# Optimization experiments

Hardware: AMD Instinct MI355X
Metric: run time of the kernel (lower is better)

## Reference

```python
import jax, jax.numpy as jnp
import numpy as np

NEG_SLOPE = 0.01  # nn.LeakyReLU default


def leaky_relu(x):
    return jnp.where(x >= 0, x, NEG_SLOPE * x)


def gcn_conv(x, W, b, src, dst, n_nodes):
    """PyG GCNConv: add self loops, symmetric D^-1/2 (A+I) D^-1/2 norm, then x @ W + b."""
    h = x @ W  # [N, D]
    # degree with self-loops (edge weight 1 each, +1 for the self loop)
    deg = jnp.zeros((n_nodes,), dtype=x.dtype).at[dst].add(1.0) + 1.0
    dinv = jax.lax.rsqrt(deg)  # deg >= 1 thanks to self loops
    norm = dinv[src] * dinv[dst]  # [E]
    msg = h[src] * norm[:, None]  # gather + scale, [E, D]
    agg = jnp.zeros_like(h).at[dst].add(msg)  # scatter-add over targets
    agg = agg + h * (dinv * dinv)[:, None]  # self-loop contribution
    return agg + b


def setup_inputs() -> dict:
    key = jax.random.key(0)
    ks = jax.random.split(key, 12)
    N, E = 100000, 640000
    ND, D, C = 239, 128, 2
    x = jax.random.normal(ks[0], (N, ND), dtype=jnp.float32)
    edge_index = jax.random.randint(ks[1], (2, E), 0, N, dtype=jnp.int64)
    edge_type = jax.random.randint(ks[2], (E,), 0, 4, dtype=jnp.int64)
    s = 0.05
    W_in = jax.random.normal(ks[3], (ND, D), dtype=jnp.float32) * s
    b_in = jax.random.normal(ks[4], (D,), dtype=jnp.float32) * s
    W_g = jax.random.normal(ks[5], (D, D), dtype=jnp.float32) * s
    b_g = jax.random.normal(ks[6], (D,), dtype=jnp.float32) * s
    W_o1 = jax.random.normal(ks[7], (D, D), dtype=jnp.float32) * s
    b_o1 = jax.random.normal(ks[8], (D,), dtype=jnp.float32) * s
    W_o2 = jax.random.normal(ks[9], (D, C), dtype=jnp.float32) * s
    b_o2 = jax.random.normal(ks[10], (C,), dtype=jnp.float32) * s
    return {"x": x, "edge_index": edge_index, "edge_type": edge_type,
            "W_in": W_in, "b_in": b_in, "W_g": W_g, "b_g": b_g,
            "W_o1": W_o1, "b_o1": b_o1, "W_o2": W_o2, "b_o2": b_o2}


def reference(x, edge_index, edge_type, W_in, b_in, W_g, b_g, W_o1, b_o1, W_o2, b_o2):
    n_nodes = x.shape[0]
    src, dst = edge_index[0], edge_index[1]
    h = leaky_relu(x @ W_in + b_in)
    h = gcn_conv(h, W_g, b_g, src, dst, n_nodes)
    # dropout is identity in eval mode (training=False)
    h = gcn_conv(h, W_g, b_g, src, dst, n_nodes)  # same shared GCNConv instance
    h = leaky_relu(h @ W_o1 + b_o1)
    return h @ W_o2 + b_o2
```

## Files before the change

kernel.cpp:

```cpp
#include <hip/hip_runtime.h>
#include <hip/hip_bf16.h>


typedef __attribute__((ext_vector_type(8))) __bf16 bf16x8;
typedef __attribute__((ext_vector_type(4))) float f32x4;

typedef __attribute__((address_space(1))) const void gvoid_t;
typedef __attribute__((address_space(3))) void svoid_t;

__global__ __launch_bounds__(256) void wtr_all_k(const float* __restrict__ W_in,
                                                 const float* __restrict__ W_g,
                                                 const float* __restrict__ W_o1,
                                                 ushort* __restrict__ Wt_in,
                                                 ushort* __restrict__ Wt_g,
                                                 ushort* __restrict__ Wt_o1, int ND) {
  int idx = blockIdx.x * 256 + threadIdx.x;
  if (idx < 128 * 256) {
    int n = idx >> 8, k = idx & 255;
    float v = (k < ND) ? W_in[(size_t)k * 128 + n] : 0.f;
    __hip_bfloat16 h = __float2bfloat16(v);
    Wt_in[idx] = *(ushort*)&h;
  } else if (idx < 128 * 256 + 128 * 128) {
    int j = idx - 128 * 256;
    int n = j >> 7, k = j & 127;
    __hip_bfloat16 h = __float2bfloat16(W_g[(size_t)k * 128 + n]);
    Wt_g[j] = *(ushort*)&h;
  } else if (idx < 128 * 256 + 2 * 128 * 128) {
    int j = idx - 128 * 256 - 128 * 128;
    int n = j >> 7, k = j & 127;
    __hip_bfloat16 h = __float2bfloat16(W_o1[(size_t)k * 128 + n]);
    Wt_o1[j] = *(ushort*)&h;
  }
}


__global__ __launch_bounds__(256) void zero_k(int* __restrict__ p, int n) {
  int i = blockIdx.x * 256 + threadIdx.x;
  if (i < n) p[i] = 0;
}

__global__ __launch_bounds__(256) void hist_k(const int* __restrict__ dst, int* __restrict__ cnt, int E) {
  int e = blockIdx.x * 256 + threadIdx.x;
  if (e < E) atomicAdd(&cnt[dst[e]], 1);
}

__global__ __launch_bounds__(256) void scan1_k(const int* __restrict__ cnt, int* __restrict__ rp,
                                               int* __restrict__ bsum, int N) {
  __shared__ int sd[256];
  int t = threadIdx.x;
  int base = blockIdx.x * 1024 + t * 4;
  int v0 = (base + 0 < N) ? cnt[base + 0] : 0;
  int v1 = (base + 1 < N) ? cnt[base + 1] : 0;
  int v2 = (base + 2 < N) ? cnt[base + 2] : 0;
  int v3 = (base + 3 < N) ? cnt[base + 3] : 0;
  int ts = v0 + v1 + v2 + v3;
  sd[t] = ts;
  __syncthreads();
  for (int off = 1; off < 256; off <<= 1) {
    int y = (t >= off) ? sd[t - off] : 0;
    __syncthreads();
    sd[t] += y;
    __syncthreads();
  }
  int x = sd[t] - ts;
  if (t == 255) bsum[blockIdx.x] = sd[255];
  if (base + 0 < N) rp[base + 0] = x; x += v0;
  if (base + 1 < N) rp[base + 1] = x; x += v1;
  if (base + 2 < N) rp[base + 2] = x; x += v2;
  if (base + 3 < N) rp[base + 3] = x;
}

__global__ __launch_bounds__(256) void scan2_k(int* __restrict__ bsum, int NB) {
  __shared__ int sd[256];
  int t = threadIdx.x;
  int base = t * 4;
  int v0 = (base + 0 < NB) ? bsum[base + 0] : 0;
  int v1 = (base + 1 < NB) ? bsum[base + 1] : 0;
  int v2 = (base + 2 < NB) ? bsum[base + 2] : 0;
  int v3 = (base + 3 < NB) ? bsum[base + 3] : 0;
  int ts = v0 + v1 + v2 + v3;
  sd[t] = ts;
  __syncthreads();
  for (int off = 1; off < 256; off <<= 1) {
    int y = (t >= off) ? sd[t - off] : 0;
    __syncthreads();
    sd[t] += y;
    __syncthreads();
  }
  int x = sd[t] - ts;
  if (base + 0 < NB) bsum[base + 0] = x; x += v0;
  if (base + 1 < NB) bsum[base + 1] = x; x += v1;
  if (base + 2 < NB) bsum[base + 2] = x; x += v2;
  if (base + 3 < NB) bsum[base + 3] = x;
}

__global__ __launch_bounds__(256) void scan3_k(int* __restrict__ rp, int* __restrict__ pos,
                                               const int* __restrict__ bsum,
                                               float* __restrict__ dinv, int N, int E) {
  int i = blockIdx.x * 256 + threadIdx.x;
  if (i < N) {
    int c = pos[i];
    int v = rp[i] + bsum[i >> 10];
    dinv[i] = rsqrtf((float)c + 1.0f);
    rp[i] = v;
    pos[i] = v;
  }
  if (i == 0) rp[N] = E;
}

__global__ __launch_bounds__(256) void fill_k(const int* __restrict__ src, const int* __restrict__ dst,
                                              const float* __restrict__ dinv,
                                              int* __restrict__ pos, int2* __restrict__ ew, int E) {
  int e = blockIdx.x * 256 + threadIdx.x;
  if (e < E) {
    int d = dst[e];
    int s = src[e];
    int idx = atomicAdd(&pos[d], 1);
    ew[idx] = make_int2(s, __float_as_int(dinv[s] * dinv[d]));
  }
}


__global__ __launch_bounds__(512, 4) void gemm1_k(const float* __restrict__ x,
                                                  const ushort* __restrict__ Wt,
                                                  const float* __restrict__ bias,
                                                  ushort* __restrict__ C, int N, int Ka) {
  __shared__ float Af[64 * 239 + 8];
  __shared__ ushort Wl[128 * 72];
  const int tid = threadIdx.x;
  const int wave = tid >> 6;
  const int lane = tid & 63;
  const int l16 = lane & 15;
  const int quad = lane >> 4;
  const int m0 = blockIdx.x * 64;

  {
    int rows = N - m0;
    if (rows > 64) rows = 64;
    const int nwords = rows * Ka;
    const float* __restrict__ gsrc = x + (size_t)m0 * Ka;
    const int nchunks = nwords >> 8;
    for (int ch = wave; ch < nchunks; ch += 8) {
      __builtin_amdgcn_global_load_lds(
          (gvoid_t*)(gsrc + ch * 256 + lane * 4),
          (svoid_t*)(&Af[ch * 256]), 16, 0, 0);
    }
    for (int i = (nchunks << 8) + tid; i < nwords; i += 512) {
      Af[i] = gsrc[i];
    }
  }

  f32x4 acc[4] = {};
  const int wr = wave >> 1;
  const int wc = wave & 1;
  const int wn = tid >> 2;
  const int wseg = tid & 3;
#pragma unroll
  for (int kc = 0; kc < 4; ++kc) {
    __syncthreads();
    *(uint4*)&Wl[wn * 72 + wseg * 16] =
        *(const uint4*)(Wt + (size_t)wn * 256 + kc * 64 + wseg * 16);
    *(uint4*)&Wl[wn * 72 + wseg * 16 + 8] =
        *(const uint4*)(Wt + (size_t)wn * 256 + kc * 64 + wseg * 16 + 8);
    __syncthreads();
#pragma unroll
    for (int s = 0; s < 2; ++s) {
      const int koff = kc * 64 + s * 32 + quad * 8;
      bf16x8 a = {};
      const float* ap = &Af[(wr * 16 + l16) * Ka + koff];
      if (koff + 8 <= Ka) {
#pragma unroll
        for (int j = 0; j < 8; ++j) {
          __hip_bfloat16 h = __float2bfloat16(ap[j]);
          a[j] = *(__bf16*)&h;
        }
      } else if (koff < Ka) {
#pragma unroll
        for (int j = 0; j < 8; ++j) {
          if (koff + j < Ka) {
            __hip_bfloat16 h = __float2bfloat16(ap[j]);
            a[j] = *(__bf16*)&h;
          }
        }
      }
      const int wof = s * 32 + quad * 8;
#pragma unroll
      for (int c = 0; c < 4; ++c) {
        bf16x8 b = *(const bf16x8*)&Wl[(wc * 64 + c * 16 + l16) * 72 + wof];
        acc[c] = __builtin_amdgcn_mfma_f32_16x16x32_bf16(a, b, acc[c], 0, 0, 0);
      }
    }
  }

  float bv[4];
#pragma unroll
  for (int c = 0; c < 4; ++c) bv[c] = bias[wc * 64 + c * 16 + l16];
#pragma unroll
  for (int reg = 0; reg < 4; ++reg) {
    int row = m0 + wr * 16 + quad * 4 + reg;
    if (row < N) {
#pragma unroll
      for (int c = 0; c < 4; ++c) {
        float v = acc[c][reg] + bv[c];
        v = v >= 0.f ? v : 0.01f * v;
        __hip_bfloat16 h = __float2bfloat16(v);
        C[(size_t)row * 128 + wc * 64 + c * 16 + l16] = *(ushort*)&h;
      }
    }
  }
}


template <int MODE>
__global__ __launch_bounds__(512, 4) void mgemm_k(const ushort* __restrict__ A,
                                                  const ushort* __restrict__ Wt,
                                                  const float* __restrict__ bias,
                                                  const float* __restrict__ W2,
                                                  const float* __restrict__ b2,
                                                  void* __restrict__ C, int N) {
  __shared__ uint4 Al[128 * 16];
  __shared__ uint4 Wl[128 * 16];
  const int tid = threadIdx.x;
  const int wave = tid >> 6;
  const int lane = tid & 63;
  const int l16 = lane & 15;
  const int quad = lane >> 4;
  const int m0 = blockIdx.x * 128;

  f32x4 acc[8] = {};
  const int r_s = tid >> 4;
  const int j8 = tid & 15;
#pragma unroll
  for (int it = 0; it < 4; ++it) {
    int m = it * 32 + r_s;
    Al[m * 16 + (j8 ^ (m & 15))] = *(const uint4*)(A + (size_t)(m0 + m) * 128 + j8 * 8);
  }
#pragma unroll
  for (int it = 0; it < 4; ++it) {
    int n = it * 32 + r_s;
    Wl[n * 16 + (j8 ^ (n & 15))] = *(const uint4*)(Wt + (size_t)n * 128 + j8 * 8);
  }
  __syncthreads();
#pragma unroll
  for (int s = 0; s < 4; ++s) {
    const int j = s * 4 + quad;
    const int arow = wave * 16 + l16;
    bf16x8 a = *(const bf16x8*)&Al[arow * 16 + (j ^ (arow & 15))];
#pragma unroll
    for (int c = 0; c < 8; ++c) {
      const int brow = c * 16 + l16;
      bf16x8 b = *(const bf16x8*)&Wl[brow * 16 + (j ^ (brow & 15))];
      acc[c] = __builtin_amdgcn_mfma_f32_16x16x32_bf16(a, b, acc[c], 0, 0, 0);
    }
  }

  float bv[8];
#pragma unroll
  for (int c = 0; c < 8; ++c) bv[c] = bias[c * 16 + l16];

  if constexpr (MODE == 3) {
    float w20[8], w21[8];
#pragma unroll
    for (int c = 0; c < 8; ++c) {
      int colj = c * 16 + l16;
      w20[c] = W2[colj * 2 + 0];
      w21[c] = W2[colj * 2 + 1];
    }
    float bb0 = b2[0], bb1 = b2[1];
#pragma unroll
    for (int reg = 0; reg < 4; ++reg) {
      float o0 = 0.f, o1 = 0.f;
#pragma unroll
      for (int c = 0; c < 8; ++c) {
        float v = acc[c][reg] + bv[c];
        v = v >= 0.f ? v : 0.01f * v;
        o0 = fmaf(v, w20[c], o0);
        o1 = fmaf(v, w21[c], o1);
      }
      o0 += __shfl_xor(o0, 1); o0 += __shfl_xor(o0, 2);
      o0 += __shfl_xor(o0, 4); o0 += __shfl_xor(o0, 8);
      o1 += __shfl_xor(o1, 1); o1 += __shfl_xor(o1, 2);
      o1 += __shfl_xor(o1, 4); o1 += __shfl_xor(o1, 8);
      int row = m0 + wave * 16 + quad * 4 + reg;
      if (l16 == 0 && row < N)
        *(float2*)((float*)C + (size_t)row * 2) = make_float2(o0 + bb0, o1 + bb1);
    }
    return;
  }

#pragma unroll
  for (int reg = 0; reg < 4; ++reg) {
    int row = m0 + wave * 16 + quad * 4 + reg;
    if (row < N) {
#pragma unroll
      for (int c = 0; c < 8; ++c) {
        float v = acc[c][reg] + bv[c];
        __hip_bfloat16 h = __float2bfloat16(v);
        ((ushort*)C)[(size_t)row * 128 + c * 16 + l16] = *(ushort*)&h;
      }
    }
  }
}


__global__ __launch_bounds__(256) void agg_k(const ushort* __restrict__ T,
                                             const float* __restrict__ dinv,
                                             const int* __restrict__ rp,
                                             const int2* __restrict__ ew,
                                             ushort* __restrict__ O, int N) {
  int l = threadIdx.x & 15;
  int node = blockIdx.x * 16 + (threadIdx.x >> 4);
  if (node >= N) return;
  float di = dinv[node];
  float dsq = di * di;
  const uint4* T4 = (const uint4*)T;
  float a[8];
  {
    uint4 sv = T4[(size_t)node * 16 + l];
    uint u[4] = {sv.x, sv.y, sv.z, sv.w};
#pragma unroll
    for (int p = 0; p < 4; ++p) {
      a[2 * p + 0] = __uint_as_float(u[p] << 16) * dsq;
      a[2 * p + 1] = __uint_as_float(u[p] & 0xFFFF0000u) * dsq;
    }
  }
  int e = rp[node];
  const int e1 = rp[node + 1];
  for (; e + 4 <= e1; e += 4) {
    int2 p0 = ew[e + 0], p1 = ew[e + 1], p2 = ew[e + 2], p3 = ew[e + 3];
    uint4 v0 = T4[(size_t)p0.x * 16 + l];
    uint4 v1 = T4[(size_t)p1.x * 16 + l];
    uint4 v2 = T4[(size_t)p2.x * 16 + l];
    uint4 v3 = T4[(size_t)p3.x * 16 + l];
    float w0 = __int_as_float(p0.y), w1 = __int_as_float(p1.y);
    float w2 = __int_as_float(p2.y), w3 = __int_as_float(p3.y);
    uint u0[4] = {v0.x, v0.y, v0.z, v0.w};
    uint u1[4] = {v1.x, v1.y, v1.z, v1.w};
    uint u2[4] = {v2.x, v2.y, v2.z, v2.w};
    uint u3[4] = {v3.x, v3.y, v3.z, v3.w};
#pragma unroll
    for (int p = 0; p < 4; ++p) {
      a[2 * p + 0] = fmaf(__uint_as_float(u0[p] << 16), w0, a[2 * p + 0]);
      a[2 * p + 1] = fmaf(__uint_as_float(u0[p] & 0xFFFF0000u), w0, a[2 * p + 1]);
      a[2 * p + 0] = fmaf(__uint_as_float(u1[p] << 16), w1, a[2 * p + 0]);
      a[2 * p + 1] = fmaf(__uint_as_float(u1[p] & 0xFFFF0000u), w1, a[2 * p + 1]);
      a[2 * p + 0] = fmaf(__uint_as_float(u2[p] << 16), w2, a[2 * p + 0]);
      a[2 * p + 1] = fmaf(__uint_as_float(u2[p] & 0xFFFF0000u), w2, a[2 * p + 1]);
      a[2 * p + 0] = fmaf(__uint_as_float(u3[p] << 16), w3, a[2 * p + 0]);
      a[2 * p + 1] = fmaf(__uint_as_float(u3[p] & 0xFFFF0000u), w3, a[2 * p + 1]);
    }
  }
  if (e + 2 <= e1) {
    int2 p0 = ew[e + 0], p1 = ew[e + 1];
    uint4 v0 = T4[(size_t)p0.x * 16 + l];
    uint4 v1 = T4[(size_t)p1.x * 16 + l];
    float w0 = __int_as_float(p0.y), w1 = __int_as_float(p1.y);
    uint u0[4] = {v0.x, v0.y, v0.z, v0.w};
    uint u1[4] = {v1.x, v1.y, v1.z, v1.w};
#pragma unroll
    for (int p = 0; p < 4; ++p) {
      a[2 * p + 0] = fmaf(__uint_as_float(u0[p] << 16), w0, a[2 * p + 0]);
      a[2 * p + 1] = fmaf(__uint_as_float(u0[p] & 0xFFFF0000u), w0, a[2 * p + 1]);
      a[2 * p + 0] = fmaf(__uint_as_float(u1[p] << 16), w1, a[2 * p + 0]);
      a[2 * p + 1] = fmaf(__uint_as_float(u1[p] & 0xFFFF0000u), w1, a[2 * p + 1]);
    }
    e += 2;
  }
  if (e < e1) {
    int2 pw = ew[e];
    float w = __int_as_float(pw.y);
    uint4 v = T4[(size_t)pw.x * 16 + l];
    uint u[4] = {v.x, v.y, v.z, v.w};
#pragma unroll
    for (int p = 0; p < 4; ++p) {
      a[2 * p + 0] = fmaf(__uint_as_float(u[p] << 16), w, a[2 * p + 0]);
      a[2 * p + 1] = fmaf(__uint_as_float(u[p] & 0xFFFF0000u), w, a[2 * p + 1]);
    }
  }
  union { uint4 v; ushort s[8]; } uo;
#pragma unroll
  for (int j = 0; j < 8; ++j) {
    __hip_bfloat16 h = __float2bfloat16(a[j]);
    uo.s[j] = *(ushort*)&h;
  }
  ((uint4*)O)[(size_t)node * 16 + l] = uo.v;
}


extern "C" void kernel_launch(void* const* d_in, const int* in_sizes, int n_in,
                              void* d_out, int out_size, void* d_ws, size_t ws_size,
                              hipStream_t stream) {
  const float* x = (const float*)d_in[0];
  const int* ei = (const int*)d_in[1];
  const float* W_in = (const float*)d_in[3];
  const float* b_in = (const float*)d_in[4];
  const float* W_g  = (const float*)d_in[5];
  const float* b_g  = (const float*)d_in[6];
  const float* W_o1 = (const float*)d_in[7];
  const float* b_o1 = (const float*)d_in[8];
  const float* W_o2 = (const float*)d_in[9];
  const float* b_o2 = (const float*)d_in[10];

  const int D = in_sizes[4];
  const int ND = in_sizes[3] / D;
  const int N = in_sizes[0] / ND;
  const int E = in_sizes[2];
  const int* src = ei;
  const int* dst = ei + E;

  const int N_pad = ((N + 127) / 128) * 128;
  const size_t np = (size_t)N_pad;
  const int KP1 = 256;

  ushort* hA = (ushort*)d_ws;
  ushort* hB = hA + np * 128;
  ushort* Wt_in = hB + np * 128;
  ushort* Wt_g  = Wt_in + 128 * 256;
  ushort* Wt_o1 = Wt_g + 128 * 128;
  float* dinv = (float*)(Wt_o1 + 128 * 128);
  int* cnt  = (int*)(dinv + N);
  int* rp   = cnt + N;
  int* bsum = rp + (N + 1);
  int2* ew  = (int2*)(((size_t)(bsum + 1024) + 7) & ~(size_t)7);

  const int NB = (N + 1023) / 1024;

  wtr_all_k<<<(128 * KP1 + 2 * 128 * 128 + 255) / 256, 256, 0, stream>>>(
      W_in, W_g, W_o1, Wt_in, Wt_g, Wt_o1, ND);

  zero_k<<<(N + 255) / 256, 256, 0, stream>>>(cnt, N);
  hist_k<<<(E + 255) / 256, 256, 0, stream>>>(dst, cnt, E);
  scan1_k<<<NB, 256, 0, stream>>>(cnt, rp, bsum, N);
  scan2_k<<<1, 256, 0, stream>>>(bsum, NB);
  scan3_k<<<(N + 255) / 256, 256, 0, stream>>>(rp, cnt , bsum, dinv, N, E);
  fill_k<<<(E + 255) / 256, 256, 0, stream>>>(src, dst, dinv, cnt, ew, E);

  const int g1blocks = (N + 63) / 64;
  const int gblocks = N_pad / 128;
  const int ablocks = (N + 15) / 16;
  gemm1_k<<<g1blocks, 512, 0, stream>>>(x, Wt_in, b_in, hA, N, ND);
  agg_k<<<ablocks, 256, 0, stream>>>(hA, dinv, rp, ew, hB, N);
  mgemm_k<1><<<gblocks, 512, 0, stream>>>(hB, Wt_g, b_g, nullptr, nullptr, hA, N);
  agg_k<<<ablocks, 256, 0, stream>>>(hA, dinv, rp, ew, hB, N);
  mgemm_k<1><<<gblocks, 512, 0, stream>>>(hB, Wt_g, b_g, nullptr, nullptr, hA, N);
  mgemm_k<3><<<gblocks, 512, 0, stream>>>(hA, Wt_o1, b_o1, W_o2, b_o2, d_out, N);
}
```

Before: 347.4 us.

## Restructure input GEMM: stage full weight in swizzled LDS, load x rows directly

The first GEMM now loads the whole 128x256 bf16 weight into LDS once per block, using an XOR swizzle to avoid bank conflicts. The x tile is no longer staged through LDS: each lane reads its fp32 rows straight from global memory as unaligned float4 loads and converts them to bf16 in registers. Blocks now cover 128 rows, two 16-row MFMA tiles per wave, which halves the block count and the per-block weight traffic and drops the per-K-chunk syncs. The cost is 64KB of LDS per block, which limits occupancy, and uncoalesced strided global reads of x. The tail handling for K=239 is special-cased with overlapping loads.

Measured after the change: 362.8 us. 1.04x slower.

```diff
diff --git a/kernel.cpp b/kernel.cpp
--- a/kernel.cpp
+++ b/kernel.cpp
@@ -4,9 +4,7 @@
 
 typedef __attribute__((ext_vector_type(8))) __bf16 bf16x8;
 typedef __attribute__((ext_vector_type(4))) float f32x4;
-
-typedef __attribute__((address_space(1))) const void gvoid_t;
-typedef __attribute__((address_space(3))) void svoid_t;
+typedef float f32x4u __attribute__((ext_vector_type(4), aligned(4)));
 
 __global__ __launch_bounds__(256) void wtr_all_k(const float* __restrict__ W_in,
                                                  const float* __restrict__ W_g,
@@ -121,90 +119,98 @@
 }
 
 
+__device__ __forceinline__ bf16x8 cvt8(f32x4u lo, f32x4u hi) {
+  bf16x8 r;
+#pragma unroll
+  for (int j = 0; j < 4; ++j) {
+    __hip_bfloat16 h = __float2bfloat16(lo[j]);
+    r[j] = *(__bf16*)&h;
+  }
+#pragma unroll
+  for (int j = 0; j < 4; ++j) {
+    __hip_bfloat16 h = __float2bfloat16(hi[j]);
+    r[4 + j] = *(__bf16*)&h;
+  }
+  return r;
+}
+
 __global__ __launch_bounds__(512, 4) void gemm1_k(const float* __restrict__ x,
                                                   const ushort* __restrict__ Wt,
                                                   const float* __restrict__ bias,
                                                   ushort* __restrict__ C, int N, int Ka) {
-  __shared__ float Af[64 * 239 + 8];
-  __shared__ ushort Wl[128 * 72];
+  __shared__ char Wb[65536];
   const int tid = threadIdx.x;
   const int wave = tid >> 6;
   const int lane = tid & 63;
   const int l16 = lane & 15;
   const int quad = lane >> 4;
-  const int m0 = blockIdx.x * 64;
-
-  {
-    int rows = N - m0;
-    if (rows > 64) rows = 64;
-    const int nwords = rows * Ka;
-    const float* __restrict__ gsrc = x + (size_t)m0 * Ka;
-    const int nchunks = nwords >> 8;
-    for (int ch = wave; ch < nchunks; ch += 8) {
-      __builtin_amdgcn_global_load_lds(
-          (gvoid_t*)(gsrc + ch * 256 + lane * 4),
-          (svoid_t*)(&Af[ch * 256]), 16, 0, 0);
-    }
-    for (int i = (nchunks << 8) + tid; i < nwords; i += 512) {
-      Af[i] = gsrc[i];
-    }
-  }
-
-  f32x4 acc[4] = {};
+  const int m0 = blockIdx.x * 128;
   const int wr = wave >> 1;
   const int wc = wave & 1;
-  const int wn = tid >> 2;
-  const int wseg = tid & 3;
-#pragma unroll
-  for (int kc = 0; kc < 4; ++kc) {
-    __syncthreads();
-    *(uint4*)&Wl[wn * 72 + wseg * 16] =
-        *(const uint4*)(Wt + (size_t)wn * 256 + kc * 64 + wseg * 16);
-    *(uint4*)&Wl[wn * 72 + wseg * 16 + 8] =
-        *(const uint4*)(Wt + (size_t)wn * 256 + kc * 64 + wseg * 16 + 8);
-    __syncthreads();
-#pragma unroll
-    for (int s = 0; s < 2; ++s) {
-      const int koff = kc * 64 + s * 32 + quad * 8;
-      bf16x8 a = {};
-      const float* ap = &Af[(wr * 16 + l16) * Ka + koff];
-      if (koff + 8 <= Ka) {
-#pragma unroll
-        for (int j = 0; j < 8; ++j) {
-          __hip_bfloat16 h = __float2bfloat16(ap[j]);
-          a[j] = *(__bf16*)&h;
+
+#pragma unroll
+  for (int it = 0; it < 8; ++it) {
+    int f = it * 512 + tid;
+    int row = f >> 5, c32 = f & 31;
+    uint4 v = *(const uint4*)(Wt + (size_t)row * 256 + c32 * 8);
+    int ofs = (row * 512 + c32 * 16) ^ ((row & 7) << 4);
+    *(uint4*)(Wb + ofs) = v;
+  }
+  __syncthreads();
+
+  int rA0 = m0 + wr * 32 + l16;
+  int rA1 = rA0 + 16;
+  if (rA0 > N - 1) rA0 = N - 1;
+  if (rA1 > N - 1) rA1 = N - 1;
+  const float* __restrict__ xr0 = x + (size_t)rA0 * Ka;
+  const float* __restrict__ xr1 = x + (size_t)rA1 * Ka;
+
+  f32x4 acc[2][4] = {};
+
+#pragma unroll
+  for (int t = 0; t < 8; ++t) {
+    const int k0 = t * 32 + quad * 8;
+    bf16x8 a0, a1;
+    if (t < 7 || quad == 0) {
+      a0 = cvt8(*(const f32x4u*)(xr0 + k0), *(const f32x4u*)(xr0 + k0 + 4));
+      a1 = cvt8(*(const f32x4u*)(xr1 + k0), *(const f32x4u*)(xr1 + k0 + 4));
+    } else if (quad == 1) {
+      f32x4u lo0 = *(const f32x4u*)(xr0 + 232), hi0 = *(const f32x4u*)(xr0 + 235);
+      f32x4u lo1 = *(const f32x4u*)(xr1 + 232), hi1 = *(const f32x4u*)(xr1 + 235);
+      f32x4u h0 = {hi0[1], hi0[2], hi0[3], 0.f};
+      f32x4u h1 = {hi1[1], hi1[2], hi1[3], 0.f};
+      a0 = cvt8(lo0, h0);
+      a1 = cvt8(lo1, h1);
+    } else {
+      a0 = bf16x8{};
+      a1 = bf16x8{};
+    }
+    const int kb = t * 64 + quad * 16;
+#pragma unroll
+    for (int c = 0; c < 4; ++c) {
+      const int brow = wc * 64 + c * 16 + l16;
+      bf16x8 b = *(const bf16x8*)(Wb + ((brow * 512 + kb) ^ ((brow & 7) << 4)));
+      acc[0][c] = __builtin_amdgcn_mfma_f32_16x16x32_bf16(a0, b, acc[0][c], 0, 0, 0);
+      acc[1][c] = __builtin_amdgcn_mfma_f32_16x16x32_bf16(a1, b, acc[1][c], 0, 0, 0);
+    }
+  }
+
+  float bv[4];
+#pragma unroll
+  for (int c = 0; c < 4; ++c) bv[c] = bias[wc * 64 + c * 16 + l16];
+#pragma unroll
+  for (int rt = 0; rt < 2; ++rt) {
+#pragma unroll
+    for (int reg = 0; reg < 4; ++reg) {
+      int row = m0 + wr * 32 + rt * 16 + quad * 4 + reg;
+      if (row < N) {
+#pragma unroll
+        for (int c = 0; c < 4; ++c) {
+          float v = acc[rt][c][reg] + bv[c];
+          v = v >= 0.f ? v : 0.01f * v;
+          __hip_bfloat16 h = __float2bfloat16(v);
+          C[(size_t)row * 128 + wc * 64 + c * 16 + l16] = *(ushort*)&h;
         }
-      } else if (koff < Ka) {
-#pragma unroll
-        for (int j = 0; j < 8; ++j) {
-          if (koff + j < Ka) {
-            __hip_bfloat16 h = __float2bfloat16(ap[j]);
-            a[j] = *(__bf16*)&h;
-          }
-        }
-      }
-      const int wof = s * 32 + quad * 8;
-#pragma unroll
-      for (int c = 0; c < 4; ++c) {
-        bf16x8 b = *(const bf16x8*)&Wl[(wc * 64 + c * 16 + l16) * 72 + wof];
-        acc[c] = __builtin_amdgcn_mfma_f32_16x16x32_bf16(a, b, acc[c], 0, 0, 0);
-      }
-    }
-  }
-
-  float bv[4];
-#pragma unroll
-  for (int c = 0; c < 4; ++c) bv[c] = bias[wc * 64 + c * 16 + l16];
-#pragma unroll
-  for (int reg = 0; reg < 4; ++reg) {
-    int row = m0 + wr * 16 + quad * 4 + reg;
-    if (row < N) {
-#pragma unroll
-      for (int c = 0; c < 4; ++c) {
-        float v = acc[c][reg] + bv[c];
-        v = v >= 0.f ? v : 0.01f * v;
-        __hip_bfloat16 h = __float2bfloat16(v);
-        C[(size_t)row * 128 + wc * 64 + c * 16 + l16] = *(ushort*)&h;
       }
     }
   }
@@ -435,10 +441,9 @@
   scan3_k<<<(N + 255) / 256, 256, 0, stream>>>(rp, cnt , bsum, dinv, N, E);
   fill_k<<<(E + 255) / 256, 256, 0, stream>>>(src, dst, dinv, cnt, ew, E);
 
-  const int g1blocks = (N + 63) / 64;
   const int gblocks = N_pad / 128;
   const int ablocks = (N + 15) / 16;
-  gemm1_k<<<g1blocks, 512, 0, stream>>>(x, Wt_in, b_in, hA, N, ND);
+  gemm1_k<<<gblocks, 512, 0, stream>>>(x, Wt_in, b_in, hA, N, ND);
   agg_k<<<ablocks, 256, 0, stream>>>(hA, dinv, rp, ew, hB, N);
   mgemm_k<1><<<gblocks, 512, 0, stream>>>(hB, Wt_g, b_g, nullptr, nullptr, hA, N);
   agg_k<<<ablocks, 256, 0, stream>>>(hA, dinv, rp, ew, hB, N);
```

## Pre-convert input features to bf16 and use swizzled-LDS bf16 GEMM for layer one

Applied to the files above, without the earlier changes.

Adds a separate kernel that converts x from fp32 to a zero-padded bf16 buffer with 256 columns. The first GEMM is then rewritten to load bf16 tiles into XOR-swizzled LDS, using 128-row blocks and 8 MFMA columns per wave. This removes the large fp32 LDS staging and the per-element conversion inside the GEMM, which should improve occupancy. The cost is an extra pass that writes and re-reads an intermediate bf16 copy of x.

New measurement: 360.8 us. +3.8%, slower.

```diff
diff --git a/kernel.cpp b/kernel.cpp
--- a/kernel.cpp
+++ b/kernel.cpp
@@ -4,9 +4,7 @@
 
 typedef __attribute__((ext_vector_type(8))) __bf16 bf16x8;
 typedef __attribute__((ext_vector_type(4))) float f32x4;
-
-typedef __attribute__((address_space(1))) const void gvoid_t;
-typedef __attribute__((address_space(3))) void svoid_t;
+typedef float f32x4u __attribute__((ext_vector_type(4), aligned(4)));
 
 __global__ __launch_bounds__(256) void wtr_all_k(const float* __restrict__ W_in,
                                                  const float* __restrict__ W_g,
@@ -34,6 +32,45 @@
 }
 
 
+__global__ __launch_bounds__(256) void cvt_k(const float* __restrict__ x,
+                                             ushort* __restrict__ xb,
+                                             int N, int Ka) {
+  const int total = N * 32;
+  const int stride = gridDim.x * 256;
+  for (int o = blockIdx.x * 256 + threadIdx.x; o < total; o += stride) {
+    const int r = o >> 5, j = o & 31;
+    const int k0 = j * 8;
+    union { uint4 v; ushort s[8]; } out;
+    if (k0 + 8 <= Ka) {
+      const float* p = x + (size_t)r * Ka + k0;
+      f32x4u lo = *(const f32x4u*)p;
+      f32x4u hi = *(const f32x4u*)(p + 4);
+#pragma unroll
+      for (int t = 0; t < 4; ++t) {
+        __hip_bfloat16 h = __float2bfloat16(lo[t]);
+        out.s[t] = *(ushort*)&h;
+      }
+#pragma unroll
+      for (int t = 0; t < 4; ++t) {
+        __hip_bfloat16 h = __float2bfloat16(hi[t]);
+        out.s[4 + t] = *(ushort*)&h;
+      }
+    } else if (k0 < Ka) {
+      const float* p = x + (size_t)r * Ka;
+#pragma unroll
+      for (int t = 0; t < 8; ++t) {
+        float v = (k0 + t < Ka) ? p[k0 + t] : 0.f;
+        __hip_bfloat16 h = __float2bfloat16(v);
+        out.s[t] = *(ushort*)&h;
+      }
+    } else {
+      out.v = make_uint4(0, 0, 0, 0);
+    }
+    ((uint4*)xb)[o] = out.v;
+  }
+}
+
+
 __global__ __launch_bounds__(256) void zero_k(int* __restrict__ p, int n) {
   int i = blockIdx.x * 256 + threadIdx.x;
   if (i < n) p[i] = 0;
@@ -121,90 +158,65 @@
 }
 
 
-__global__ __launch_bounds__(512, 4) void gemm1_k(const float* __restrict__ x,
-                                                  const ushort* __restrict__ Wt,
-                                                  const float* __restrict__ bias,
-                                                  ushort* __restrict__ C, int N, int Ka) {
-  __shared__ float Af[64 * 239 + 8];
-  __shared__ ushort Wl[128 * 72];
+__global__ __launch_bounds__(512, 4) void gemm1b_k(const ushort* __restrict__ A,
+                                                   const ushort* __restrict__ Wt,
+                                                   const float* __restrict__ bias,
+                                                   ushort* __restrict__ C, int N) {
+  __shared__ uint4 Al[128 * 16];
+  __shared__ uint4 Wl[128 * 16];
   const int tid = threadIdx.x;
   const int wave = tid >> 6;
   const int lane = tid & 63;
   const int l16 = lane & 15;
   const int quad = lane >> 4;
-  const int m0 = blockIdx.x * 64;
-
-  {
-    int rows = N - m0;
-    if (rows > 64) rows = 64;
-    const int nwords = rows * Ka;
-    const float* __restrict__ gsrc = x + (size_t)m0 * Ka;
-    const int nchunks = nwords >> 8;
-    for (int ch = wave; ch < nchunks; ch += 8) {
-      __builtin_amdgcn_global_load_lds(
-          (gvoid_t*)(gsrc + ch * 256 + lane * 4),
-          (svoid_t*)(&Af[ch * 256]), 16, 0, 0);
-    }
-    for (int i = (nchunks << 8) + tid; i < nwords; i += 512) {
-      Af[i] = gsrc[i];
-    }
-  }
-
-  f32x4 acc[4] = {};
-  const int wr = wave >> 1;
-  const int wc = wave & 1;
-  const int wn = tid >> 2;
-  const int wseg = tid & 3;
-#pragma unroll
-  for (int kc = 0; kc < 4; ++kc) {
+  const int m0 = blockIdx.x * 128;
+
+  f32x4 acc[8] = {};
+  const int r_s = tid >> 4;
+  const int j8 = tid & 15;
+#pragma unroll
+  for (int kc = 0; kc < 2; ++kc) {
+    if (kc) __syncthreads();
+#pragma unroll
+    for (int it = 0; it < 4; ++it) {
+      int m = it * 32 + r_s;
+      Al[m * 16 + (j8 ^ (m & 15))] =
+          *(const uint4*)(A + (size_t)(m0 + m) * 256 + kc * 128 + j8 * 8);
+    }
+#pragma unroll
+    for (int it = 0; it < 4; ++it) {
+      int n = it * 32 + r_s;
+      Wl[n * 16 + (j8 ^ (n & 15))] =
+          *(const uint4*)(Wt + (size_t)n * 256 + kc * 128 + j8 * 8);
+    }
     __syncthreads();
-    *(uint4*)&Wl[wn * 72 + wseg * 16] =
-        *(const uint4*)(Wt + (size_t)wn * 256 + kc * 64 + wseg * 16);
-    *(uint4*)&Wl[wn * 72 + wseg * 16 + 8] =
-        *(const uint4*)(Wt + (size_t)wn * 256 + kc * 64 + wseg * 16 + 8);
-    __syncthreads();
-#pragma unroll
-    for (int s = 0; s < 2; ++s) {
-      const int koff = kc * 64 + s * 32 + quad * 8;
-      bf16x8 a = {};
-      const float* ap = &Af[(wr * 16 + l16) * Ka + koff];
-      if (koff + 8 <= Ka) {
-#pragma unroll
-        for (int j = 0; j < 8; ++j) {
-          __hip_bfloat16 h = __float2bfloat16(ap[j]);
-          a[j] = *(__bf16*)&h;
-        }
-      } else if (koff < Ka) {
-#pragma unroll
-        for (int j = 0; j < 8; ++j) {
-          if (koff + j < Ka) {
-            __hip_bfloat16 h = __float2bfloat16(ap[j]);
-            a[j] = *(__bf16*)&h;
-          }
-        }
-      }
-      const int wof = s * 32 + quad * 8;
-#pragma unroll
-      for (int c = 0; c < 4; ++c) {
-        bf16x8 b = *(const bf16x8*)&Wl[(wc * 64 + c * 16 + l16) * 72 + wof];
+#pragma unroll
+    for (int s = 0; s < 4; ++s) {
+      const int j = s * 4 + quad;
+      const int arow = wave * 16 + l16;
+      bf16x8 a = *(const bf16x8*)&Al[arow * 16 + (j ^ (arow & 15))];
+#pragma unroll
+      for (int c = 0; c < 8; ++c) {
+        const int brow = c * 16 + l16;
+        bf16x8 b = *(const bf16x8*)&Wl[brow * 16 + (j ^ (brow & 15))];
         acc[c] = __builtin_amdgcn_mfma_f32_16x16x32_bf16(a, b, acc[c], 0, 0, 0);
       }
     }
   }
 
-  float bv[4];
-#pragma unroll
-  for (int c = 0; c < 4; ++c) bv[c] = bias[wc * 64 + c * 16 + l16];
+  float bv[8];
+#pragma unroll
+  for (int c = 0; c < 8; ++c) bv[c] = bias[c * 16 + l16];
 #pragma unroll
   for (int reg = 0; reg < 4; ++reg) {
-    int row = m0 + wr * 16 + quad * 4 + reg;
+    int row = m0 + wave * 16 + quad * 4 + reg;
     if (row < N) {
 #pragma unroll
-      for (int c = 0; c < 4; ++c) {
+      for (int c = 0; c < 8; ++c) {
         float v = acc[c][reg] + bv[c];
         v = v >= 0.f ? v : 0.01f * v;
         __hip_bfloat16 h = __float2bfloat16(v);
-        C[(size_t)row * 128 + wc * 64 + c * 16 + l16] = *(ushort*)&h;
+        C[(size_t)row * 128 + c * 16 + l16] = *(ushort*)&h;
       }
     }
   }
@@ -412,7 +424,8 @@
   const size_t np = (size_t)N_pad;
   const int KP1 = 256;
 
-  ushort* hA = (ushort*)d_ws;
+  ushort* xb = (ushort*)d_ws;
+  ushort* hA = xb + np * 256;
   ushort* hB = hA + np * 128;
   ushort* Wt_in = hB + np * 128;
   ushort* Wt_g  = Wt_in + 128 * 256;
@@ -428,6 +441,10 @@
   wtr_all_k<<<(128 * KP1 + 2 * 128 * 128 + 255) / 256, 256, 0, stream>>>(
       W_in, W_g, W_o1, Wt_in, Wt_g, Wt_o1, ND);
 
+  int cblocks = (N * 32 + 255) / 256;
+  if (cblocks > 2048) cblocks = 2048;
+  cvt_k<<<cblocks, 256, 0, stream>>>(x, xb, N, ND);
+
   zero_k<<<(N + 255) / 256, 256, 0, stream>>>(cnt, N);
   hist_k<<<(E + 255) / 256, 256, 0, stream>>>(dst, cnt, E);
   scan1_k<<<NB, 256, 0, stream>>>(cnt, rp, bsum, N);
@@ -435,10 +452,9 @@
   scan3_k<<<(N + 255) / 256, 256, 0, stream>>>(rp, cnt , bsum, dinv, N, E);
   fill_k<<<(E + 255) / 256, 256, 0, stream>>>(src, dst, dinv, cnt, ew, E);
 
-  const int g1blocks = (N + 63) / 64;
   const int gblocks = N_pad / 128;
   const int ablocks = (N + 15) / 16;
-  gemm1_k<<<g1blocks, 512, 0, stream>>>(x, Wt_in, b_in, hA, N, ND);
+  gemm1b_k<<<gblocks, 512, 0, stream>>>(xb, Wt_in, b_in, hA, N);
   agg_k<<<ablocks, 256, 0, stream>>>(hA, dinv, rp, ew, hB, N);
   mgemm_k<1><<<gblocks, 512, 0, stream>>>(hB, Wt_g, b_g, nullptr, nullptr, hA, N);
   agg_k<<<ablocks, 256, 0, stream>>>(hA, dinv, rp, ew, hB, N);
```

## Fold count zeroing into weight prep and histogram into first GEMM launch

Applied to the files above, without the earlier changes.

Zeroing of the degree counters moves into the weight-transpose kernel, and the degree histogram is appended as extra blocks of the first input GEMM kernel. This removes two kernel launches and lets the atomic histogram run alongside the GEMM instead of serially before it. In exchange, the histogram blocks run with a 512-thread, high-LDS block configuration, which may limit how many of them are resident at once, and the first GEMM now sits ahead of the scan in the dependency chain.

Measured after the change: 336.3 us. 3.2% less time.

```diff
diff --git a/kernel.cpp b/kernel.cpp
--- a/kernel.cpp
+++ b/kernel.cpp
@@ -13,7 +13,8 @@
                                                  const float* __restrict__ W_o1,
                                                  ushort* __restrict__ Wt_in,
                                                  ushort* __restrict__ Wt_g,
-                                                 ushort* __restrict__ Wt_o1, int ND) {
+                                                 ushort* __restrict__ Wt_o1,
+                                                 int* __restrict__ cnt, int N, int ND) {
   int idx = blockIdx.x * 256 + threadIdx.x;
   if (idx < 128 * 256) {
     int n = idx >> 8, k = idx & 255;
@@ -30,19 +31,12 @@
     int n = j >> 7, k = j & 127;
     __hip_bfloat16 h = __float2bfloat16(W_o1[(size_t)k * 128 + n]);
     Wt_o1[j] = *(ushort*)&h;
-  }
-}
-
-
-__global__ __launch_bounds__(256) void zero_k(int* __restrict__ p, int n) {
-  int i = blockIdx.x * 256 + threadIdx.x;
-  if (i < n) p[i] = 0;
-}
-
-__global__ __launch_bounds__(256) void hist_k(const int* __restrict__ dst, int* __restrict__ cnt, int E) {
-  int e = blockIdx.x * 256 + threadIdx.x;
-  if (e < E) atomicAdd(&cnt[dst[e]], 1);
-}
+  } else {
+    int i = idx - 65536;
+    if (i < N) cnt[i] = 0;
+  }
+}
+
 
 __global__ __launch_bounds__(256) void scan1_k(const int* __restrict__ cnt, int* __restrict__ rp,
                                                int* __restrict__ bsum, int N) {
@@ -121,13 +115,23 @@
 }
 
 
-__global__ __launch_bounds__(512, 4) void gemm1_k(const float* __restrict__ x,
-                                                  const ushort* __restrict__ Wt,
-                                                  const float* __restrict__ bias,
-                                                  ushort* __restrict__ C, int N, int Ka) {
+__global__ __launch_bounds__(512, 4) void gemm1h_k(const float* __restrict__ x,
+                                                   const ushort* __restrict__ Wt,
+                                                   const float* __restrict__ bias,
+                                                   ushort* __restrict__ C, int N, int Ka,
+                                                   int g1b,
+                                                   const int* __restrict__ dst,
+                                                   int* __restrict__ cnt, int E) {
   __shared__ float Af[64 * 239 + 8];
   __shared__ ushort Wl[128 * 72];
   const int tid = threadIdx.x;
+
+  if (blockIdx.x >= g1b) {
+    int e = (blockIdx.x - g1b) * 512 + tid;
+    if (e < E) atomicAdd(&cnt[dst[e]], 1);
+    return;
+  }
+
   const int wave = tid >> 6;
   const int lane = tid & 63;
   const int l16 = lane & 15;
@@ -410,7 +414,6 @@
 
   const int N_pad = ((N + 127) / 128) * 128;
   const size_t np = (size_t)N_pad;
-  const int KP1 = 256;
 
   ushort* hA = (ushort*)d_ws;
   ushort* hB = hA + np * 128;
@@ -425,20 +428,21 @@
 
   const int NB = (N + 1023) / 1024;
 
-  wtr_all_k<<<(128 * KP1 + 2 * 128 * 128 + 255) / 256, 256, 0, stream>>>(
-      W_in, W_g, W_o1, Wt_in, Wt_g, Wt_o1, ND);
-
-  zero_k<<<(N + 255) / 256, 256, 0, stream>>>(cnt, N);
-  hist_k<<<(E + 255) / 256, 256, 0, stream>>>(dst, cnt, E);
+  wtr_all_k<<<(65536 + N + 255) / 256, 256, 0, stream>>>(
+      W_in, W_g, W_o1, Wt_in, Wt_g, Wt_o1, cnt, N, ND);
+
+  const int g1blocks = (N + 63) / 64;
+  const int hblocks = (E + 511) / 512;
+  gemm1h_k<<<g1blocks + hblocks, 512, 0, stream>>>(
+      x, Wt_in, b_in, hA, N, ND, g1blocks, dst, cnt, E);
+
   scan1_k<<<NB, 256, 0, stream>>>(cnt, rp, bsum, N);
   scan2_k<<<1, 256, 0, stream>>>(bsum, NB);
   scan3_k<<<(N + 255) / 256, 256, 0, stream>>>(rp, cnt , bsum, dinv, N, E);
   fill_k<<<(E + 255) / 256, 256, 0, stream>>>(src, dst, dinv, cnt, ew, E);
 
-  const int g1blocks = (N + 63) / 64;
   const int gblocks = N_pad / 128;
   const int ablocks = (N + 15) / 16;
-  gemm1_k<<<g1blocks, 512, 0, stream>>>(x, Wt_in, b_in, hA, N, ND);
   agg_k<<<ablocks, 256, 0, stream>>>(hA, dinv, rp, ew, hB, N);
   mgemm_k<1><<<gblocks, 512, 0, stream>>>(hB, Wt_g, b_g, nullptr, nullptr, hA, N);
   agg_k<<<ablocks, 256, 0, stream>>>(hA, dinv, rp, ew, hB, N);
```
